# Kernel optimization log

Hardware: AMD Instinct MI355X
Metric: run time of the kernel (lower is better)

The kernel has to match this reference:

```python
import jax, jax.numpy as jnp
import numpy as np

R = 3                 # search_radius
S2 = (2 * R + 1) ** 2  # 49 correlation channels
VIS_PIXEL_SCALE = 0.1  # arcsec / pixel


def _interp_tokens(tokens, sh, sw, dh, dw):
    # tokens [B, N, D] on (sh, sw) grid -> (dh, dw) grid
    B, N, D = tokens.shape
    x = jnp.transpose(tokens, (0, 2, 1)).reshape(B, D, sh, sw)
    if (sh, sw) != (dh, dw):
        # torch F.interpolate bilinear align_corners=False == jax half-pixel bilinear
        x = jax.image.resize(x, (B, D, dh, dw), method='bilinear')
    return x  # [B, D, dh, dw]


def _l2norm(x, eps=1e-12):
    n = jnp.sqrt(jnp.sum(x * x, axis=1, keepdims=True))
    return x / jnp.maximum(n, eps)


def _corr_volume(q, ref):
    # q, ref: [B, D, H, W]; local cosine-similarity volume [B, S2, H, W]
    q = _l2norm(q)
    ref = _l2norm(ref)
    B, D, H, W = q.shape
    refp = jnp.pad(ref, ((0, 0), (0, 0), (R, R), (R, R)), mode='edge')  # replicate pad
    slices = [
        jnp.sum(q * jax.lax.dynamic_slice(refp, (0, 0, R + dy, R + dx), (B, D, H, W)), axis=1)
        for dy in range(-R, R + 1) for dx in range(-R, R + 1)
    ]
    return jnp.stack(slices, axis=1)


def _conv5(x, w, b):
    y = jax.lax.conv_general_dilated(x, w, (1, 1), 'SAME',
                                     dimension_numbers=('NCHW', 'OIHW', 'NCHW'))
    return y + b[None, :, None, None]


def _refine_net(x, w0, b0, w1, b1, w2, b2):
    h = jax.nn.gelu(_conv5(x, w0, b0), approximate=False)
    h = jax.nn.gelu(_conv5(h, w1, b1), approximate=False)
    return _conv5(h, w2, b2)


def setup_inputs() -> dict:
    key = jax.random.key(0)
    ks = jax.random.split(key, 8)
    B, D = 4, 256
    rubin_tokens = jax.random.normal(ks[0], (B, 64 * 64, D), dtype=jnp.float32)
    vis_tokens = jax.random.normal(ks[1], (B, 128 * 128, D), dtype=jnp.float32)
    in_ch = 2 + S2 + 1  # 52
    hid = 32
    def kaiming(k, shape):
        fan_in = shape[1] * shape[2] * shape[3]
        return jax.random.normal(k, shape, dtype=jnp.float32) / np.sqrt(fan_in)
    w0 = kaiming(ks[2], (hid, in_ch, 5, 5)); b0 = jnp.zeros((hid,), jnp.float32)
    w1 = kaiming(ks[3], (hid, hid, 5, 5));   b1 = jnp.zeros((hid,), jnp.float32)
    w2 = kaiming(ks[4], (2, hid, 5, 5));     b2 = jnp.zeros((2,), jnp.float32)
    log_temp = jnp.asarray(np.log(0.1), dtype=jnp.float32)
    return {
        'rubin_tokens': rubin_tokens, 'vis_tokens': vis_tokens,
        'w0': w0, 'b0': b0, 'w1': w1, 'b1': b1, 'w2': w2, 'b2': b2,
        'log_temp': log_temp,
        'rubin_h': 64, 'rubin_w': 64, 'vis_h': 128, 'vis_w': 128,
        'img_h': 2048, 'img_w': 2048,
    }


def reference(rubin_tokens, vis_tokens, w0, b0, w1, b1, w2, b2, log_temp,
              rubin_h, rubin_w, vis_h, vis_w, img_h, img_w):
    Hc, Wc = max(rubin_h, vis_h), max(rubin_w, vis_w)
    q = _interp_tokens(rubin_tokens, rubin_h, rubin_w, Hc, Wc)  # [B,D,Hc,Wc]
    k = _interp_tokens(vis_tokens, vis_h, vis_w, Hc, Wc)
    corr = _corr_volume(q, k)  # [B,S2,Hc,Wc]

    # soft-argmax over the (2R+1)^2 neighborhood
    coords = jnp.arange(-R, R + 1, dtype=corr.dtype)
    cy, cx = jnp.meshgrid(coords, coords, indexing='ij')
    cy = cy.reshape(1, S2, 1, 1)
    cx = cx.reshape(1, S2, 1, 1)
    temp = jnp.exp(log_temp)
    weights = jax.nn.softmax(corr / temp, axis=1)
    dy = jnp.sum(weights * cy, axis=1, keepdims=True)
    dx = jnp.sum(weights * cx, axis=1, keepdims=True)
    confidence = jnp.max(weights, axis=1, keepdims=True)
    raw_offsets = jnp.concatenate([dy, dx], axis=1)  # [B,2,Hc,Wc]

    x = jnp.concatenate([raw_offsets, corr, confidence], axis=1)  # [B,52,Hc,Wc]
    residual = _refine_net(x, w0, b0, w1, b1, w2, b2)
    refined = raw_offsets + residual

    sky_per_token_y = img_h * VIS_PIXEL_SCALE / Hc
    sky_per_token_x = img_w * VIS_PIXEL_SCALE / Wc
    dra = refined[:, 1:2] * sky_per_token_x
    ddec = refined[:, 0:1] * sky_per_token_y
    # [B,5,Hc,Wc]: dra, ddec, raw_dy, raw_dx, confidence
    return jnp.concatenate([dra, ddec, dy, dx, confidence], axis=1)
```

## Files before the change

kernel.cpp:

```cpp
#include <hip/hip_runtime.h>
#include <math.h>

#define Hh 128
#define Ww 128
#define Dd 256
#define Bb 4
#define HW (Hh*Ww)
#define NPIX (Bb*HW)
#define WP 132

typedef __attribute__((ext_vector_type(8))) short s16x8;
typedef __attribute__((ext_vector_type(4))) float f32x4;

__device__ __forceinline__ unsigned short f2bf(float f) {
    unsigned u = __float_as_uint(f);
    u += 0x7FFF + ((u >> 16) & 1);
    return (unsigned short)(u >> 16);
}

__device__ __forceinline__ float gelu_exact(float v) {
    return 0.5f * v * (1.0f + erff(v * 0.70710678118654752f));
}

#define ZGRAN 1115136
__global__ __launch_bounds__(256) void setup_fill(const float* __restrict__ w0,
                                                  const float* __restrict__ w1,
                                                  const float* __restrict__ w2,
                                                  unsigned short* __restrict__ wb0,
                                                  unsigned short* __restrict__ wb1,
                                                  unsigned short* __restrict__ wb2,
                                                  uint4* __restrict__ zbase) {
    int t = blockIdx.x * 256 + threadIdx.x;
    if (t < ZGRAN) {
        zbase[t] = (uint4){0, 0, 0, 0};
        return;
    }
    int u = t - ZGRAN;
    if (u < 51200) {
        int tap = u >> 11; int r = u & 2047; int n = r >> 6; int k = r & 63;
        wb0[u] = (k < 52) ? f2bf(w0[n * 1300 + k * 25 + tap]) : (unsigned short)0;
    } else if (u < 76800) {
        int v = u - 51200; int tap = v >> 10; int r = v & 1023; int n = r >> 5; int k = r & 31;
        wb1[v] = f2bf(w1[n * 800 + k * 25 + tap]);
    } else if (u < 89600) {
        int v = u - 76800; int tap = v >> 9; int r = v & 511; int n = r >> 5; int k = r & 31;
        wb2[v] = (n < 2) ? f2bf(w2[n * 800 + k * 25 + tap]) : (unsigned short)0;
    }
}

__global__ __launch_bounds__(256) void norm_fused(const float* __restrict__ vis,
                                                  const float* __restrict__ rub,
                                                  unsigned short* __restrict__ kn,
                                                  unsigned short* __restrict__ qn) {
    int tid = threadIdx.x;
    int g16 = tid >> 4, l = tid & 15;
    int blk = blockIdx.x;
    if (blk < 4096) {
        int pix = blk * 16 + g16;
        const float* base = vis + (size_t)pix * Dd + l * 4;
        float4 v[4];
#pragma unroll
        for (int i = 0; i < 4; i++) v[i] = *(const float4*)(base + i * 64);
        float ss = 0.f;
#pragma unroll
        for (int i = 0; i < 4; i++)
            ss += v[i].x * v[i].x + v[i].y * v[i].y + v[i].z * v[i].z + v[i].w * v[i].w;
#pragma unroll
        for (int o = 1; o <= 8; o <<= 1) ss += __shfl_xor(ss, o, 64);
        float inv = __builtin_amdgcn_rsqf(fmaxf(ss, 1e-24f));
        unsigned short* op = kn + (size_t)pix * Dd + l * 4;
#pragma unroll
        for (int i = 0; i < 4; i++) {
            ushort4 o4;
            o4.x = f2bf(v[i].x * inv); o4.y = f2bf(v[i].y * inv);
            o4.z = f2bf(v[i].z * inv); o4.w = f2bf(v[i].w * inv);
            *(ushort4*)(op + i * 64) = o4;
        }
    } else {
        int pix = (blk - 4096) * 16 + g16;
        int b = pix >> 14; int yx = pix & 16383; int y = yx >> 7; int x = yx & 127;
        float sy = 0.5f * y - 0.25f;
        float sx = 0.5f * x - 0.25f;
        int y0 = (int)floorf(sy); float fy = sy - (float)y0;
        int x0 = (int)floorf(sx); float fx = sx - (float)x0;
        int y0c = max(y0, 0), y1c = min(y0 + 1, 63);
        int x0c = max(x0, 0), x1c = min(x0 + 1, 63);
        const float* base = rub + (size_t)b * 4096 * Dd + l * 4;
        const float* p00 = base + (size_t)(y0c * 64 + x0c) * Dd;
        const float* p01 = base + (size_t)(y0c * 64 + x1c) * Dd;
        const float* p10 = base + (size_t)(y1c * 64 + x0c) * Dd;
        const float* p11 = base + (size_t)(y1c * 64 + x1c) * Dd;
        float w00 = (1.f - fy) * (1.f - fx), w01 = (1.f - fy) * fx;
        float w10 = fy * (1.f - fx), w11 = fy * fx;
        float4 bv[4];
        float ss = 0.f;
#pragma unroll
        for (int i = 0; i < 4; i++) {
            float4 a = *(const float4*)(p00 + i * 64);
            float4 b1 = *(const float4*)(p01 + i * 64);
            float4 c = *(const float4*)(p10 + i * 64);
            float4 d = *(const float4*)(p11 + i * 64);
            float4 v;
            v.x = w00 * a.x + w01 * b1.x + w10 * c.x + w11 * d.x;
            v.y = w00 * a.y + w01 * b1.y + w10 * c.y + w11 * d.y;
            v.z = w00 * a.z + w01 * b1.z + w10 * c.z + w11 * d.z;
            v.w = w00 * a.w + w01 * b1.w + w10 * c.w + w11 * d.w;
            bv[i] = v;
            ss += v.x * v.x + v.y * v.y + v.z * v.z + v.w * v.w;
        }
#pragma unroll
        for (int o = 1; o <= 8; o <<= 1) ss += __shfl_xor(ss, o, 64);
        float inv = __builtin_amdgcn_rsqf(fmaxf(ss, 1e-24f));
        unsigned short* op = qn + (size_t)pix * Dd + l * 4;
#pragma unroll
        for (int i = 0; i < 4; i++) {
            ushort4 o4;
            o4.x = f2bf(bv[i].x * inv); o4.y = f2bf(bv[i].y * inv);
            o4.z = f2bf(bv[i].z * inv); o4.w = f2bf(bv[i].w * inv);
            *(ushort4*)(op + i * 64) = o4;
        }
    }
}

__global__ __launch_bounds__(1024) void corr_block(const unsigned short* __restrict__ qn,
                                                   const unsigned short* __restrict__ kn,
                                                   const float* __restrict__ log_temp,
                                                   unsigned short* __restrict__ xb,
                                                   float* __restrict__ out) {
    __shared__ char smem[484 * 5 * 16];
    int tid = threadIdx.x;
    int wid = tid >> 6, lane = tid & 63, l15 = lane & 15, quad = lane >> 4;
    int blk = blockIdx.x;
    int b = blk >> 6, rem = blk & 63;
    int y0 = ((rem >> 3) & 7) << 4, x0 = (rem & 7) << 4;
    int y = y0 + wid;

    const unsigned short* src0; int dst0;
    const unsigned short* src1 = nullptr; int dst1 = 0;
    bool hav1;
    {
        int g = tid;
        int px = g >> 2, sub = g & 3;
        int ry = px / 22, rx = px - ry * 22;
        int yy = min(max(y0 - 3 + ry, 0), 127);
        int xx = min(max(x0 - 3 + rx, 0), 127);
        src0 = kn + ((size_t)(b << 14) + yy * 128 + xx) * 256 + sub * 8;
        dst0 = (px * 5 + sub) * 16;
        g = 1024 + tid;
        hav1 = (g < 1936);
        int gc = hav1 ? g : 1935;
        px = gc >> 2; sub = gc & 3;
        ry = px / 22; rx = px - ry * 22;
        yy = min(max(y0 - 3 + ry, 0), 127);
        xx = min(max(x0 - 3 + rx, 0), 127);
        src1 = kn + ((size_t)(b << 14) + yy * 128 + xx) * 256 + sub * 8;
        dst1 = (px * 5 + sub) * 16;
    }
    int lpixoff[10];
#pragma unroll
    for (int f = 0; f < 10; f++) {
        int p = min(f * 16 + l15, 153);
        int pr = p / 22, pc = p - pr * 22;
        lpixoff[f] = (((wid + pr) * 22 + pc) * 5 + quad) * 16;
    }
    const unsigned short* aptr = qn + ((size_t)(b << 14) + y * 128 + x0 + l15) * 256 + quad * 8;

    f32x4 acc[10];
#pragma unroll
    for (int f = 0; f < 10; f++) acc[f] = (f32x4){0.f, 0.f, 0.f, 0.f};

    uint4 v0 = *(const uint4*)src0;
    uint4 v1 = *(const uint4*)src1;
    s16x8 an = *(const s16x8*)aptr;
    for (int c = 0; c < 8; c++) {
        uint4 w0v = v0, w1v = v1;
        s16x8 a = an;
        if (c < 7) {
            v0 = *(const uint4*)(src0 + (c + 1) * 32);
            v1 = *(const uint4*)(src1 + (c + 1) * 32);
            an = *(const s16x8*)(aptr + (c + 1) * 32);
        }
        __syncthreads();
        *(uint4*)(smem + dst0) = w0v;
        if (hav1) *(uint4*)(smem + dst1) = w1v;
        __syncthreads();
#pragma unroll
        for (int f = 0; f < 10; f++) {
            s16x8 bf = *(const s16x8*)(smem + lpixoff[f]);
            acc[f] = __builtin_amdgcn_mfma_f32_16x16x32_bf16(a, bf, acc[f], 0, 0, 0);
        }
    }

    float inv_temp = expf(-log_temp[0]);
    float vmax[4] = {-1e30f, -1e30f, -1e30f, -1e30f};
#pragma unroll
    for (int f = 0; f < 10; f++) {
        int n = f * 16 + l15;
        if (n <= 153) {
            int dy = n / 22 - 3;
            int rx = n - (dy + 3) * 22;
#pragma unroll
            for (int i = 0; i < 4; i++) {
                int m = quad * 4 + i;
                int dx = rx - m - 3;
                if ((unsigned)(dx + 3) <= 6u) vmax[i] = fmaxf(vmax[i], acc[f][i]);
            }
        }
    }
#pragma unroll
    for (int o = 1; o <= 8; o <<= 1) {
#pragma unroll
        for (int i = 0; i < 4; i++) vmax[i] = fmaxf(vmax[i], __shfl_xor(vmax[i], o, 64));
    }
    float se[4] = {0, 0, 0, 0}, sey[4] = {0, 0, 0, 0}, sex[4] = {0, 0, 0, 0}, emax[4] = {0, 0, 0, 0};
    unsigned short* xrow = xb + ((size_t)(b * WP + y + 2) * WP + x0 + 2) * 64;
#pragma unroll
    for (int f = 0; f < 10; f++) {
        int n = f * 16 + l15;
        if (n <= 153) {
            int dy = n / 22 - 3;
            int rx = n - (dy + 3) * 22;
#pragma unroll
            for (int i = 0; i < 4; i++) {
                int m = quad * 4 + i;
                int dx = rx - m - 3;
                if ((unsigned)(dx + 3) <= 6u) {
                    float v = acc[f][i];
                    float e = expf((v - vmax[i]) * inv_temp);
                    se[i] += e;
                    sey[i] += e * (float)dy;
                    sex[i] += e * (float)dx;
                    emax[i] = fmaxf(emax[i], e);
                    xrow[(size_t)m * 64 + 2 + (dy + 3) * 7 + (dx + 3)] = f2bf(v);
                }
            }
        }
    }
#pragma unroll
    for (int o = 1; o <= 8; o <<= 1) {
#pragma unroll
        for (int i = 0; i < 4; i++) {
            se[i] += __shfl_xor(se[i], o, 64);
            sey[i] += __shfl_xor(sey[i], o, 64);
            sex[i] += __shfl_xor(sex[i], o, 64);
            emax[i] = fmaxf(emax[i], __shfl_xor(emax[i], o, 64));
        }
    }
    if (l15 == 0) {
#pragma unroll
        for (int i = 0; i < 4; i++) {
            int m = quad * 4 + i;
            float inv_se = 1.0f / se[i];
            float dyv = sey[i] * inv_se, dxv = sex[i] * inv_se, conf = emax[i] * inv_se;
            unsigned short* xp = xrow + (size_t)m * 64;
            xp[0] = f2bf(dyv); xp[1] = f2bf(dxv); xp[51] = f2bf(conf);
            float* op = out + (size_t)b * 5 * HW + y * 128 + x0 + m;
            op[2 * HW] = dyv; op[3 * HW] = dxv; op[4 * HW] = conf;
        }
    }
}

template <int KS, int OC, bool GELU>
__global__ __launch_bounds__(1024) void conv_tile(const unsigned short* __restrict__ in,
                                                  const unsigned short* __restrict__ wb,
                                                  const float* __restrict__ bias,
                                                  unsigned short* __restrict__ outp) {
    constexpr int ICP = KS * 32;
    constexpr int NF = OC / 16;
    constexpr int ABYTES = 400 * 5 * 16;
    constexpr int WBYTES = 5 * OC * 5 * 16;
    __shared__ char smem[ABYTES + WBYTES];
    int tid = threadIdx.x;
    int wv = tid >> 6, lane = tid & 63, l15 = lane & 15, quad = lane >> 4;
    int blk = blockIdx.x;
    int b = blk >> 6, ty = (blk >> 3) & 7, tx = blk & 7;
    int y0 = ty * 16, x0 = tx * 16;

    f32x4 acc[NF];
#pragma unroll
    for (int g = 0; g < NF; g++) acc[g] = (f32x4){0.f, 0.f, 0.f, 0.f};

    for (int ks = 0; ks < KS; ks++) {
        __syncthreads();
#pragma unroll
        for (int i = 0; i < 2; i++) {
            int g = i * 1024 + tid;
            if (g < 1600) {
                int px = g >> 2, sub = g & 3;
                int r = px / 20, c = px - r * 20;
                *(uint4*)(smem + (px * 5 + sub) * 16) =
                    *(const uint4*)(in + ((size_t)(b * WP + y0 + r) * WP + x0 + c) * ICP + ks * 32 + sub * 8);
            }
        }
        for (int ky = 0; ky < 5; ky++) {
            if (ky > 0) __syncthreads();
            constexpr int WGR = 5 * OC * 4;
#pragma unroll
            for (int i = 0; i < (WGR + 1023) / 1024; i++) {
                int g = i * 1024 + tid;
                if (g < WGR) {
                    int nl = g >> 2, sub = g & 3;
                    *(uint4*)(smem + ABYTES + (nl * 5 + sub) * 16) =
                        *(const uint4*)(wb + ((size_t)(ky * 5 * OC) + nl) * ICP + ks * 32 + sub * 8);
                }
            }
            __syncthreads();
#pragma unroll
            for (int kx = 0; kx < 5; kx++) {
                int abyte = (((wv + ky) * 20 + l15 + kx) * 5 + quad) * 16;
                s16x8 a = *(const s16x8*)(smem + abyte);
#pragma unroll
                for (int g = 0; g < NF; g++) {
                    int wbyte = ABYTES + ((kx * OC + g * 16 + l15) * 5 + quad) * 16;
                    s16x8 bf = *(const s16x8*)(smem + wbyte);
                    acc[g] = __builtin_amdgcn_mfma_f32_16x16x32_bf16(a, bf, acc[g], 0, 0, 0);
                }
            }
        }
    }
    size_t orow = ((size_t)(b * WP + y0 + wv + 2) * WP + x0 + 2) * OC;
#pragma unroll
    for (int g = 0; g < NF; g++) {
        float bv = bias[g * 16 + l15];
#pragma unroll
        for (int r = 0; r < 4; r++) {
            int m = quad * 4 + r;
            float v = acc[g][r] + bv;
            if (GELU) v = gelu_exact(v);
            outp[orow + (size_t)m * OC + g * 16 + l15] = f2bf(v);
        }
    }
}

__global__ __launch_bounds__(1024) void conv_final_tile(const unsigned short* __restrict__ in,
                                                        const unsigned short* __restrict__ wb,
                                                        const float* __restrict__ bias,
                                                        float* __restrict__ out) {
    constexpr int ICP = 32, OC = 16;
    constexpr int ABYTES = 400 * 5 * 16;
    constexpr int WBYTES = 5 * OC * 5 * 16;
    __shared__ char smem[ABYTES + WBYTES];
    int tid = threadIdx.x;
    int wv = tid >> 6, lane = tid & 63, l15 = lane & 15, quad = lane >> 4;
    int blk = blockIdx.x;
    int b = blk >> 6, ty = (blk >> 3) & 7, tx = blk & 7;
    int y0 = ty * 16, x0 = tx * 16;

    f32x4 acc = (f32x4){0.f, 0.f, 0.f, 0.f};
    __syncthreads();
#pragma unroll
    for (int i = 0; i < 2; i++) {
        int g = i * 1024 + tid;
        if (g < 1600) {
            int px = g >> 2, sub = g & 3;
            int r = px / 20, c = px - r * 20;
            *(uint4*)(smem + (px * 5 + sub) * 16) =
                *(const uint4*)(in + ((size_t)(b * WP + y0 + r) * WP + x0 + c) * ICP + sub * 8);
        }
    }
    for (int ky = 0; ky < 5; ky++) {
        if (ky > 0) __syncthreads();
        constexpr int WGR = 5 * OC * 4;
        {
            int g = tid;
            if (g < WGR) {
                int nl = g >> 2, sub = g & 3;
                *(uint4*)(smem + ABYTES + (nl * 5 + sub) * 16) =
                    *(const uint4*)(wb + ((size_t)(ky * 5 * OC) + nl) * ICP + sub * 8);
            }
        }
        __syncthreads();
#pragma unroll
        for (int kx = 0; kx < 5; kx++) {
            int abyte = (((wv + ky) * 20 + l15 + kx) * 5 + quad) * 16;
            s16x8 a = *(const s16x8*)(smem + abyte);
            int wbyte = ABYTES + ((kx * OC + l15) * 5 + quad) * 16;
            s16x8 bf = *(const s16x8*)(smem + wbyte);
            acc = __builtin_amdgcn_mfma_f32_16x16x32_bf16(a, bf, acc, 0, 0, 0);
        }
    }
    if (l15 < 2) {
        float bv = bias[l15];
#pragma unroll
        for (int r = 0; r < 4; r++) {
            int m = quad * 4 + r;
            size_t p5 = (size_t)b * 5 * HW + (y0 + wv) * Ww + x0 + m;
            float a = acc[r] + bv;
            if (l15 == 0) {
                float dyv = out[p5 + 2 * HW];
                out[p5 + HW] = (dyv + a) * 1.6f;
            } else {
                float dxv = out[p5 + 3 * HW];
                out[p5] = (dxv + a) * 1.6f;
            }
        }
    }
}

extern "C" void kernel_launch(void* const* d_in, const int* in_sizes, int n_in,
                              void* d_out, int out_size, void* d_ws, size_t ws_size,
                              hipStream_t stream) {
    const float* rub = (const float*)d_in[0];
    const float* vis = (const float*)d_in[1];
    const float* w0 = (const float*)d_in[2];
    const float* b0 = (const float*)d_in[3];
    const float* w1 = (const float*)d_in[4];
    const float* b1 = (const float*)d_in[5];
    const float* w2 = (const float*)d_in[6];
    const float* b2 = (const float*)d_in[7];
    const float* log_temp = (const float*)d_in[8];
    float* out = (float*)d_out;

    char* ws = (char*)d_ws;
    size_t off = 0;
    const size_t PADPIX = (size_t)Bb * WP * WP;
    unsigned short* kn = (unsigned short*)(ws + off); off += (size_t)NPIX * Dd * 2;
    unsigned short* qn = (unsigned short*)(ws + off); off += (size_t)NPIX * Dd * 2;
    unsigned short* xbp = (unsigned short*)(ws + off); off += PADPIX * 64 * 2;
    unsigned short* h1p = (unsigned short*)(ws + off); off += PADPIX * 32 * 2;
    unsigned short* h2p = (unsigned short*)(ws + off); off += PADPIX * 32 * 2;
    unsigned short* wb0 = (unsigned short*)(ws + off); off += 51200 * 2;
    unsigned short* wb1 = (unsigned short*)(ws + off); off += 25600 * 2;
    unsigned short* wb2 = (unsigned short*)(ws + off); off += 12800 * 2;

    setup_fill<<<4706, 256, 0, stream>>>(w0, w1, w2, wb0, wb1, wb2, (uint4*)xbp);
    norm_fused<<<8192, 256, 0, stream>>>(vis, rub, kn, qn);
    corr_block<<<256, 1024, 0, stream>>>(qn, kn, log_temp, xbp, out);
    conv_tile<2, 32, true><<<256, 1024, 0, stream>>>(xbp, wb0, b0, h1p);
    conv_tile<1, 32, true><<<256, 1024, 0, stream>>>(h1p, wb1, b1, h2p);
    conv_final_tile<<<256, 1024, 0, stream>>>(h2p, wb2, b2, out);
}
```

Measured before the change: 216.1 us.

## Fuse three refine convolutions into one halo-recompute pyramid kernel

Replaces the three separate conv kernels with one kernel per 16x16 tile. It loads a 28x28 halo of the correlation features, computes conv1 on 24x24 and conv2 on 20x20 in shared memory, then runs the final conv, with XOR-swizzled LDS layouts. The padded border grows from 2 to 6 so the larger halo can be read, and the h1/h2 global buffers go away. This removes two launches and the global round-trips of the intermediate activations, at the cost of recomputing halo pixels (about 2.25x the conv1 work) and much larger shared memory per block.

```diff
diff --git a/kernel.cpp b/kernel.cpp
--- a/kernel.cpp
+++ b/kernel.cpp
@@ -7,7 +7,7 @@
 #define Bb 4
 #define HW (Hh*Ww)
 #define NPIX (Bb*HW)
-#define WP 132
+#define WP 140
 
 typedef __attribute__((ext_vector_type(8))) short s16x8;
 typedef __attribute__((ext_vector_type(4))) float f32x4;
@@ -22,7 +22,7 @@
     return 0.5f * v * (1.0f + erff(v * 0.70710678118654752f));
 }
 
-#define ZGRAN 1115136
+#define ZGRAN 627200
 __global__ __launch_bounds__(256) void setup_fill(const float* __restrict__ w0,
                                                   const float* __restrict__ w1,
                                                   const float* __restrict__ w2,
@@ -213,7 +213,7 @@
         for (int i = 0; i < 4; i++) vmax[i] = fmaxf(vmax[i], __shfl_xor(vmax[i], o, 64));
     }
     float se[4] = {0, 0, 0, 0}, sey[4] = {0, 0, 0, 0}, sex[4] = {0, 0, 0, 0}, emax[4] = {0, 0, 0, 0};
-    unsigned short* xrow = xb + ((size_t)(b * WP + y + 2) * WP + x0 + 2) * 64;
+    unsigned short* xrow = xb + ((size_t)(b * WP + y + 6) * WP + x0 + 6) * 64;
 #pragma unroll
     for (int f = 0; f < 10; f++) {
         int n = f * 16 + l15;
@@ -260,138 +260,204 @@
     }
 }
 
-template <int KS, int OC, bool GELU>
-__global__ __launch_bounds__(1024) void conv_tile(const unsigned short* __restrict__ in,
-                                                  const unsigned short* __restrict__ wb,
-                                                  const float* __restrict__ bias,
-                                                  unsigned short* __restrict__ outp) {
-    constexpr int ICP = KS * 32;
-    constexpr int NF = OC / 16;
-    constexpr int ABYTES = 400 * 5 * 16;
-    constexpr int WBYTES = 5 * OC * 5 * 16;
-    __shared__ char smem[ABYTES + WBYTES];
+__global__ __launch_bounds__(1024) void conv_pyramid(const unsigned short* __restrict__ xb,
+                                                     const unsigned short* __restrict__ wb0,
+                                                     const float* __restrict__ b0,
+                                                     const unsigned short* __restrict__ wb1,
+                                                     const float* __restrict__ b1,
+                                                     const unsigned short* __restrict__ wb2,
+                                                     const float* __restrict__ b2,
+                                                     float* __restrict__ out) {
+    constexpr int XBYTES = 784 * 64;
+    constexpr int WBYTES = 13 * 32 * 64;
+    constexpr int H1BYTES = 576 * 64;
+    constexpr int H2BYTES = 400 * 64;
+    __shared__ char smem[XBYTES + WBYTES + H1BYTES + H2BYTES];
+    char* sX = smem;
+    char* sW = smem + XBYTES;
+    char* sH1 = smem + XBYTES + WBYTES;
+    char* sH2 = sH1 + H1BYTES;
+
     int tid = threadIdx.x;
     int wv = tid >> 6, lane = tid & 63, l15 = lane & 15, quad = lane >> 4;
     int blk = blockIdx.x;
     int b = blk >> 6, ty = (blk >> 3) & 7, tx = blk & 7;
     int y0 = ty * 16, x0 = tx * 16;
 
-    f32x4 acc[NF];
-#pragma unroll
-    for (int g = 0; g < NF; g++) acc[g] = (f32x4){0.f, 0.f, 0.f, 0.f};
-
-    for (int ks = 0; ks < KS; ks++) {
-        __syncthreads();
-#pragma unroll
-        for (int i = 0; i < 2; i++) {
+    auto stage_x = [&](int ks) {
+#pragma unroll
+        for (int i = 0; i < 4; i++) {
             int g = i * 1024 + tid;
-            if (g < 1600) {
+            if (g < 3136) {
                 int px = g >> 2, sub = g & 3;
-                int r = px / 20, c = px - r * 20;
-                *(uint4*)(smem + (px * 5 + sub) * 16) =
-                    *(const uint4*)(in + ((size_t)(b * WP + y0 + r) * WP + x0 + c) * ICP + ks * 32 + sub * 8);
-            }
-        }
-        for (int ky = 0; ky < 5; ky++) {
-            if (ky > 0) __syncthreads();
-            constexpr int WGR = 5 * OC * 4;
-#pragma unroll
-            for (int i = 0; i < (WGR + 1023) / 1024; i++) {
-                int g = i * 1024 + tid;
-                if (g < WGR) {
-                    int nl = g >> 2, sub = g & 3;
-                    *(uint4*)(smem + ABYTES + (nl * 5 + sub) * 16) =
-                        *(const uint4*)(wb + ((size_t)(ky * 5 * OC) + nl) * ICP + ks * 32 + sub * 8);
+                int r = px / 28, c = px - r * 28;
+                *(uint4*)(sX + px * 64 + ((sub ^ ((px >> 1) & 3)) << 4)) =
+                    *(const uint4*)(xb + ((size_t)(b * WP + y0 + r) * WP + x0 + c) * 64 + ks * 32 + sub * 8);
+            }
+        }
+    };
+    auto stage_w = [&](const unsigned short* src, int rows, int rlen, int choff) {
+        int ngr = rows * 4;
+        for (int i = 0; i * 1024 < ngr; i++) {
+            int g = i * 1024 + tid;
+            if (g < ngr) {
+                int nl = g >> 2, sub = g & 3;
+                *(uint4*)(sW + nl * 64 + ((sub ^ ((nl >> 1) & 3)) << 4)) =
+                    *(const uint4*)(src + (size_t)nl * rlen + choff + sub * 8);
+            }
+        }
+    };
+
+    f32x4 acc1[3][2];
+#pragma unroll
+    for (int s = 0; s < 3; s++) { acc1[s][0] = (f32x4){0,0,0,0}; acc1[s][1] = (f32x4){0,0,0,0}; }
+
+    auto conv1_half = [&](int tap0, int nt) {
+        for (int t = 0; t < nt; t++) {
+            int tap = tap0 + t;
+            int ky = tap / 5, kx = tap - ky * 5;
+            int lr0 = t * 32 + l15;
+            s16x8 wf0 = *(const s16x8*)(sW + lr0 * 64 + ((quad ^ ((lr0 >> 1) & 3)) << 4));
+            int lr1 = lr0 + 16;
+            s16x8 wf1 = *(const s16x8*)(sW + lr1 * 64 + ((quad ^ ((lr1 >> 1) & 3)) << 4));
+#pragma unroll
+            for (int s = 0; s < 3; s++) {
+                int u = s * 16 + wv;
+                int r = u >> 1, cb = (u & 1) << 4;
+                int px = (r + ky) * 28 + min(cb + l15 + kx, 27);
+                s16x8 a = *(const s16x8*)(sX + px * 64 + ((quad ^ ((px >> 1) & 3)) << 4));
+                acc1[s][0] = __builtin_amdgcn_mfma_f32_16x16x32_bf16(a, wf0, acc1[s][0], 0, 0, 0);
+                acc1[s][1] = __builtin_amdgcn_mfma_f32_16x16x32_bf16(a, wf1, acc1[s][1], 0, 0, 0);
+            }
+        }
+    };
+
+    stage_x(0); stage_w(wb0, 13 * 32, 64, 0);
+    __syncthreads();
+    conv1_half(0, 13);
+    __syncthreads();
+    stage_w(wb0 + 13 * 32 * 64, 12 * 32, 64, 0);
+    __syncthreads();
+    conv1_half(13, 12);
+    __syncthreads();
+    stage_x(1); stage_w(wb0, 13 * 32, 64, 32);
+    __syncthreads();
+    conv1_half(0, 13);
+    __syncthreads();
+    stage_w(wb0 + 13 * 32 * 64, 12 * 32, 64, 32);
+    __syncthreads();
+    conv1_half(13, 12);
+
+#pragma unroll
+    for (int s = 0; s < 3; s++) {
+        int u = s * 16 + wv;
+        int r = u >> 1, cb = (u & 1) << 4;
+        int ay = y0 + r - 4;
+#pragma unroll
+        for (int g = 0; g < 2; g++) {
+            float bv = b0[g * 16 + l15];
+#pragma unroll
+            for (int rr = 0; rr < 4; rr++) {
+                int col = cb + quad * 4 + rr;
+                if (col < 24) {
+                    float v = gelu_exact(acc1[s][g][rr] + bv);
+                    int ax = x0 + col - 4;
+                    unsigned short o = ((unsigned)ay < 128u && (unsigned)ax < 128u) ? f2bf(v)
+                                                                                    : (unsigned short)0;
+                    int px = r * 24 + col;
+                    int gran = g * 2 + (l15 >> 3);
+                    *(unsigned short*)(sH1 + px * 64 + ((gran ^ ((px >> 1) & 3)) << 4) + (l15 & 7) * 2) = o;
                 }
             }
-            __syncthreads();
-#pragma unroll
-            for (int kx = 0; kx < 5; kx++) {
-                int abyte = (((wv + ky) * 20 + l15 + kx) * 5 + quad) * 16;
-                s16x8 a = *(const s16x8*)(smem + abyte);
-#pragma unroll
-                for (int g = 0; g < NF; g++) {
-                    int wbyte = ABYTES + ((kx * OC + g * 16 + l15) * 5 + quad) * 16;
-                    s16x8 bf = *(const s16x8*)(smem + wbyte);
-                    acc[g] = __builtin_amdgcn_mfma_f32_16x16x32_bf16(a, bf, acc[g], 0, 0, 0);
+        }
+    }
+    __syncthreads();
+
+    f32x4 acc2[3][2];
+#pragma unroll
+    for (int s = 0; s < 3; s++) { acc2[s][0] = (f32x4){0,0,0,0}; acc2[s][1] = (f32x4){0,0,0,0}; }
+
+    auto conv2_half = [&](int tap0, int nt) {
+        for (int t = 0; t < nt; t++) {
+            int tap = tap0 + t;
+            int ky = tap / 5, kx = tap - ky * 5;
+            int lr0 = t * 32 + l15;
+            s16x8 wf0 = *(const s16x8*)(sW + lr0 * 64 + ((quad ^ ((lr0 >> 1) & 3)) << 4));
+            int lr1 = lr0 + 16;
+            s16x8 wf1 = *(const s16x8*)(sW + lr1 * 64 + ((quad ^ ((lr1 >> 1) & 3)) << 4));
+#pragma unroll
+            for (int s = 0; s < 3; s++) {
+                int u = s * 16 + wv;
+                if (u < 40) {
+                    int r = u >> 1, cb = (u & 1) << 4;
+                    int px = (r + ky) * 24 + min(cb + l15 + kx, 23);
+                    s16x8 a = *(const s16x8*)(sH1 + px * 64 + ((quad ^ ((px >> 1) & 3)) << 4));
+                    acc2[s][0] = __builtin_amdgcn_mfma_f32_16x16x32_bf16(a, wf0, acc2[s][0], 0, 0, 0);
+                    acc2[s][1] = __builtin_amdgcn_mfma_f32_16x16x32_bf16(a, wf1, acc2[s][1], 0, 0, 0);
                 }
             }
         }
-    }
-    size_t orow = ((size_t)(b * WP + y0 + wv + 2) * WP + x0 + 2) * OC;
-#pragma unroll
-    for (int g = 0; g < NF; g++) {
-        float bv = bias[g * 16 + l15];
-#pragma unroll
-        for (int r = 0; r < 4; r++) {
-            int m = quad * 4 + r;
-            float v = acc[g][r] + bv;
-            if (GELU) v = gelu_exact(v);
-            outp[orow + (size_t)m * OC + g * 16 + l15] = f2bf(v);
-        }
-    }
-}
-
-__global__ __launch_bounds__(1024) void conv_final_tile(const unsigned short* __restrict__ in,
-                                                        const unsigned short* __restrict__ wb,
-                                                        const float* __restrict__ bias,
-                                                        float* __restrict__ out) {
-    constexpr int ICP = 32, OC = 16;
-    constexpr int ABYTES = 400 * 5 * 16;
-    constexpr int WBYTES = 5 * OC * 5 * 16;
-    __shared__ char smem[ABYTES + WBYTES];
-    int tid = threadIdx.x;
-    int wv = tid >> 6, lane = tid & 63, l15 = lane & 15, quad = lane >> 4;
-    int blk = blockIdx.x;
-    int b = blk >> 6, ty = (blk >> 3) & 7, tx = blk & 7;
-    int y0 = ty * 16, x0 = tx * 16;
-
-    f32x4 acc = (f32x4){0.f, 0.f, 0.f, 0.f};
-    __syncthreads();
-#pragma unroll
-    for (int i = 0; i < 2; i++) {
-        int g = i * 1024 + tid;
-        if (g < 1600) {
-            int px = g >> 2, sub = g & 3;
-            int r = px / 20, c = px - r * 20;
-            *(uint4*)(smem + (px * 5 + sub) * 16) =
-                *(const uint4*)(in + ((size_t)(b * WP + y0 + r) * WP + x0 + c) * ICP + sub * 8);
-        }
-    }
-    for (int ky = 0; ky < 5; ky++) {
-        if (ky > 0) __syncthreads();
-        constexpr int WGR = 5 * OC * 4;
-        {
-            int g = tid;
-            if (g < WGR) {
-                int nl = g >> 2, sub = g & 3;
-                *(uint4*)(smem + ABYTES + (nl * 5 + sub) * 16) =
-                    *(const uint4*)(wb + ((size_t)(ky * 5 * OC) + nl) * ICP + sub * 8);
-            }
-        }
-        __syncthreads();
-#pragma unroll
-        for (int kx = 0; kx < 5; kx++) {
-            int abyte = (((wv + ky) * 20 + l15 + kx) * 5 + quad) * 16;
-            s16x8 a = *(const s16x8*)(smem + abyte);
-            int wbyte = ABYTES + ((kx * OC + l15) * 5 + quad) * 16;
-            s16x8 bf = *(const s16x8*)(smem + wbyte);
-            acc = __builtin_amdgcn_mfma_f32_16x16x32_bf16(a, bf, acc, 0, 0, 0);
-        }
-    }
+    };
+
+    stage_w(wb1, 13 * 32, 32, 0);
+    __syncthreads();
+    conv2_half(0, 13);
+    __syncthreads();
+    stage_w(wb1 + 13 * 32 * 32, 12 * 32, 32, 0);
+    __syncthreads();
+    conv2_half(13, 12);
+
+#pragma unroll
+    for (int s = 0; s < 3; s++) {
+        int u = s * 16 + wv;
+        if (u < 40) {
+            int r = u >> 1, cb = (u & 1) << 4;
+            int ay = y0 + r - 2;
+#pragma unroll
+            for (int g = 0; g < 2; g++) {
+                float bv = b1[g * 16 + l15];
+#pragma unroll
+                for (int rr = 0; rr < 4; rr++) {
+                    int col = cb + quad * 4 + rr;
+                    if (col < 20) {
+                        float v = gelu_exact(acc2[s][g][rr] + bv);
+                        int ax = x0 + col - 2;
+                        unsigned short o = ((unsigned)ay < 128u && (unsigned)ax < 128u) ? f2bf(v)
+                                                                                        : (unsigned short)0;
+                        int px = r * 20 + col;
+                        int gran = g * 2 + (l15 >> 3);
+                        *(unsigned short*)(sH2 + px * 64 + ((gran ^ ((px >> 1) & 3)) << 4) + (l15 & 7) * 2) = o;
+                    }
+                }
+            }
+        }
+    }
+    __syncthreads();
+
+    stage_w(wb2, 400, 32, 0);
+    __syncthreads();
+
+    f32x4 acc3 = (f32x4){0, 0, 0, 0};
+    for (int t = 0; t < 25; t++) {
+        int ky = t / 5, kx = t - ky * 5;
+        int px = (wv + ky) * 20 + l15 + kx;
+        s16x8 a = *(const s16x8*)(sH2 + px * 64 + ((quad ^ ((px >> 1) & 3)) << 4));
+        int lr = t * 16 + l15;
+        s16x8 wf = *(const s16x8*)(sW + lr * 64 + ((quad ^ ((lr >> 1) & 3)) << 4));
+        acc3 = __builtin_amdgcn_mfma_f32_16x16x32_bf16(a, wf, acc3, 0, 0, 0);
+    }
+
     if (l15 < 2) {
-        float bv = bias[l15];
-#pragma unroll
-        for (int r = 0; r < 4; r++) {
-            int m = quad * 4 + r;
+        float bv = b2[l15];
+#pragma unroll
+        for (int rr = 0; rr < 4; rr++) {
+            int m = quad * 4 + rr;
             size_t p5 = (size_t)b * 5 * HW + (y0 + wv) * Ww + x0 + m;
-            float a = acc[r] + bv;
+            float a = acc3[rr] + bv;
             if (l15 == 0) {
-                float dyv = out[p5 + 2 * HW];
-                out[p5 + HW] = (dyv + a) * 1.6f;
+                out[p5 + HW] = (out[p5 + 2 * HW] + a) * 1.6f;
             } else {
-                float dxv = out[p5 + 3 * HW];
-                out[p5] = (dxv + a) * 1.6f;
+                out[p5] = (out[p5 + 3 * HW] + a) * 1.6f;
             }
         }
     }
@@ -417,16 +483,12 @@
     unsigned short* kn = (unsigned short*)(ws + off); off += (size_t)NPIX * Dd * 2;
     unsigned short* qn = (unsigned short*)(ws + off); off += (size_t)NPIX * Dd * 2;
     unsigned short* xbp = (unsigned short*)(ws + off); off += PADPIX * 64 * 2;
-    unsigned short* h1p = (unsigned short*)(ws + off); off += PADPIX * 32 * 2;
-    unsigned short* h2p = (unsigned short*)(ws + off); off += PADPIX * 32 * 2;
     unsigned short* wb0 = (unsigned short*)(ws + off); off += 51200 * 2;
     unsigned short* wb1 = (unsigned short*)(ws + off); off += 25600 * 2;
     unsigned short* wb2 = (unsigned short*)(ws + off); off += 12800 * 2;
 
-    setup_fill<<<4706, 256, 0, stream>>>(w0, w1, w2, wb0, wb1, wb2, (uint4*)xbp);
+    setup_fill<<<2800, 256, 0, stream>>>(w0, w1, w2, wb0, wb1, wb2, (uint4*)xbp);
     norm_fused<<<8192, 256, 0, stream>>>(vis, rub, kn, qn);
     corr_block<<<256, 1024, 0, stream>>>(qn, kn, log_temp, xbp, out);
-    conv_tile<2, 32, true><<<256, 1024, 0, stream>>>(xbp, wb0, b0, h1p);
-    conv_tile<1, 32, true><<<256, 1024, 0, stream>>>(h1p, wb1, b1, h2p);
-    conv_final_tile<<<256, 1024, 0, stream>>>(h2p, wb2, b2, out);
-}
+    conv_pyramid<<<256, 1024, 0, stream>>>(xbp, wb0, b0, wb1, b1, wb2, b2, out);
+}
```

Result: slower. 248.2 us (+14.8%).

## Stage rubin tokens in LDS for upsample and halve spatial tiles across kernels

Applied to the files above, without the earlier changes.

Each rubin-upsample block now loads a 6x6 token patch (with clamped borders) into shared memory once and computes an 8x8 patch of bilinear-interpolated, normalized outputs from LDS. Before, every output pixel issued four global float4 gathers. The correlation and conv kernels switch from 16x16 tiles with 1024 threads to 8x16 tiles with 512 threads. That doubles the grid to 512 blocks so more of the CUs are busy and several blocks can share a CU. The smaller tiles add halo overhead per output pixel, and the norm kernel's new 37 KB shared buffer is also allocated by the vis-normalization blocks, which may cut their occupancy.

```diff
diff --git a/kernel.cpp b/kernel.cpp
--- a/kernel.cpp
+++ b/kernel.cpp
@@ -52,6 +52,7 @@
                                                   const float* __restrict__ rub,
                                                   unsigned short* __restrict__ kn,
                                                   unsigned short* __restrict__ qn) {
+    __shared__ float stok[36 * 260];
     int tid = threadIdx.x;
     int g16 = tid >> 4, l = tid & 15;
     int blk = blockIdx.x;
@@ -77,67 +78,85 @@
             *(ushort4*)(op + i * 64) = o4;
         }
     } else {
-        int pix = (blk - 4096) * 16 + g16;
-        int b = pix >> 14; int yx = pix & 16383; int y = yx >> 7; int x = yx & 127;
-        float sy = 0.5f * y - 0.25f;
-        float sx = 0.5f * x - 0.25f;
-        int y0 = (int)floorf(sy); float fy = sy - (float)y0;
-        int x0 = (int)floorf(sx); float fx = sx - (float)x0;
-        int y0c = max(y0, 0), y1c = min(y0 + 1, 63);
-        int x0c = max(x0, 0), x1c = min(x0 + 1, 63);
-        const float* base = rub + (size_t)b * 4096 * Dd + l * 4;
-        const float* p00 = base + (size_t)(y0c * 64 + x0c) * Dd;
-        const float* p01 = base + (size_t)(y0c * 64 + x1c) * Dd;
-        const float* p10 = base + (size_t)(y1c * 64 + x0c) * Dd;
-        const float* p11 = base + (size_t)(y1c * 64 + x1c) * Dd;
-        float w00 = (1.f - fy) * (1.f - fx), w01 = (1.f - fy) * fx;
-        float w10 = fy * (1.f - fx), w11 = fy * fx;
-        float4 bv[4];
-        float ss = 0.f;
-#pragma unroll
-        for (int i = 0; i < 4; i++) {
-            float4 a = *(const float4*)(p00 + i * 64);
-            float4 b1 = *(const float4*)(p01 + i * 64);
-            float4 c = *(const float4*)(p10 + i * 64);
-            float4 d = *(const float4*)(p11 + i * 64);
-            float4 v;
-            v.x = w00 * a.x + w01 * b1.x + w10 * c.x + w11 * d.x;
-            v.y = w00 * a.y + w01 * b1.y + w10 * c.y + w11 * d.y;
-            v.z = w00 * a.z + w01 * b1.z + w10 * c.z + w11 * d.z;
-            v.w = w00 * a.w + w01 * b1.w + w10 * c.w + w11 * d.w;
-            bv[i] = v;
-            ss += v.x * v.x + v.y * v.y + v.z * v.z + v.w * v.w;
-        }
-#pragma unroll
-        for (int o = 1; o <= 8; o <<= 1) ss += __shfl_xor(ss, o, 64);
-        float inv = __builtin_amdgcn_rsqf(fmaxf(ss, 1e-24f));
-        unsigned short* op = qn + (size_t)pix * Dd + l * 4;
-#pragma unroll
-        for (int i = 0; i < 4; i++) {
-            ushort4 o4;
-            o4.x = f2bf(bv[i].x * inv); o4.y = f2bf(bv[i].y * inv);
-            o4.z = f2bf(bv[i].z * inv); o4.w = f2bf(bv[i].w * inv);
-            *(ushort4*)(op + i * 64) = o4;
-        }
-    }
-}
-
-__global__ __launch_bounds__(1024) void corr_block(const unsigned short* __restrict__ qn,
-                                                   const unsigned short* __restrict__ kn,
-                                                   const float* __restrict__ log_temp,
-                                                   unsigned short* __restrict__ xb,
-                                                   float* __restrict__ out) {
-    __shared__ char smem[484 * 5 * 16];
+        int blk2 = blk - 4096;
+        int b = blk2 >> 8;
+        int rem = blk2 & 255;
+        int ty = rem >> 4, tx = rem & 15;
+        int oy0 = ty * 8, ox0 = tx * 8;
+        int rb = ty * 4 - 1, cb = tx * 4 - 1;
+#pragma unroll
+        for (int i = 0; i < 9; i++) {
+            int g = i * 256 + tid;
+            int t = g >> 6, c = g & 63;
+            int jy = t / 6, jx = t - jy * 6;
+            int gy = min(max(rb + jy, 0), 63);
+            int gx = min(max(cb + jx, 0), 63);
+            *(float4*)&stok[t * 260 + c * 4] =
+                *(const float4*)(rub + ((size_t)(b * 4096 + gy * 64 + gx)) * 256 + c * 4);
+        }
+        __syncthreads();
+        for (int k = 0; k < 4; k++) {
+            int pp = g16 * 4 + k;
+            int r = pp >> 3, c2 = pp & 7;
+            int yo = oy0 + r, xo = ox0 + c2;
+            float sy = 0.5f * yo - 0.25f, sx = 0.5f * xo - 0.25f;
+            float fyf = floorf(sy), fxf = floorf(sx);
+            float fy = sy - fyf, fx = sx - fxf;
+            int jy0 = (int)fyf - rb, jx0 = (int)fxf - cb;
+            const float* t00 = &stok[(jy0 * 6 + jx0) * 260 + l * 4];
+            const float* t01 = t00 + 260;
+            const float* t10 = t00 + 6 * 260;
+            const float* t11 = t10 + 260;
+            float w00 = (1.f - fy) * (1.f - fx), w01 = (1.f - fy) * fx;
+            float w10 = fy * (1.f - fx), w11 = fy * fx;
+            float4 bv[4];
+            float ss = 0.f;
+#pragma unroll
+            for (int i = 0; i < 4; i++) {
+                float4 a = *(const float4*)(t00 + i * 64);
+                float4 b1 = *(const float4*)(t01 + i * 64);
+                float4 c = *(const float4*)(t10 + i * 64);
+                float4 d = *(const float4*)(t11 + i * 64);
+                float4 v;
+                v.x = w00 * a.x + w01 * b1.x + w10 * c.x + w11 * d.x;
+                v.y = w00 * a.y + w01 * b1.y + w10 * c.y + w11 * d.y;
+                v.z = w00 * a.z + w01 * b1.z + w10 * c.z + w11 * d.z;
+                v.w = w00 * a.w + w01 * b1.w + w10 * c.w + w11 * d.w;
+                bv[i] = v;
+                ss += v.x * v.x + v.y * v.y + v.z * v.z + v.w * v.w;
+            }
+#pragma unroll
+            for (int o = 1; o <= 8; o <<= 1) ss += __shfl_xor(ss, o, 64);
+            float inv = __builtin_amdgcn_rsqf(fmaxf(ss, 1e-24f));
+            size_t pix = (size_t)(b << 14) + yo * 128 + xo;
+            unsigned short* op = qn + pix * Dd + l * 4;
+#pragma unroll
+            for (int i = 0; i < 4; i++) {
+                ushort4 o4;
+                o4.x = f2bf(bv[i].x * inv); o4.y = f2bf(bv[i].y * inv);
+                o4.z = f2bf(bv[i].z * inv); o4.w = f2bf(bv[i].w * inv);
+                *(ushort4*)(op + i * 64) = o4;
+            }
+        }
+    }
+}
+
+__global__ __launch_bounds__(512, 4) void corr_block(const unsigned short* __restrict__ qn,
+                                                     const unsigned short* __restrict__ kn,
+                                                     const float* __restrict__ log_temp,
+                                                     unsigned short* __restrict__ xb,
+                                                     float* __restrict__ out) {
+    __shared__ char smem[308 * 5 * 16];
     int tid = threadIdx.x;
     int wid = tid >> 6, lane = tid & 63, l15 = lane & 15, quad = lane >> 4;
     int blk = blockIdx.x;
-    int b = blk >> 6, rem = blk & 63;
-    int y0 = ((rem >> 3) & 7) << 4, x0 = (rem & 7) << 4;
+    int b = blk >> 7, rem = blk & 127;
+    int y0 = (rem >> 3) << 3, x0 = (rem & 7) << 4;
     int y = y0 + wid;
 
     const unsigned short* src0; int dst0;
-    const unsigned short* src1 = nullptr; int dst1 = 0;
-    bool hav1;
+    const unsigned short* src1; int dst1;
+    const unsigned short* src2; int dst2; bool hav2;
     {
         int g = tid;
         int px = g >> 2, sub = g & 3;
@@ -146,15 +165,22 @@
         int xx = min(max(x0 - 3 + rx, 0), 127);
         src0 = kn + ((size_t)(b << 14) + yy * 128 + xx) * 256 + sub * 8;
         dst0 = (px * 5 + sub) * 16;
-        g = 1024 + tid;
-        hav1 = (g < 1936);
-        int gc = hav1 ? g : 1935;
-        px = gc >> 2; sub = gc & 3;
+        g = 512 + tid;
+        px = g >> 2; sub = g & 3;
         ry = px / 22; rx = px - ry * 22;
         yy = min(max(y0 - 3 + ry, 0), 127);
         xx = min(max(x0 - 3 + rx, 0), 127);
         src1 = kn + ((size_t)(b << 14) + yy * 128 + xx) * 256 + sub * 8;
         dst1 = (px * 5 + sub) * 16;
+        g = 1024 + tid;
+        hav2 = (g < 1232);
+        int gc = hav2 ? g : 1231;
+        px = gc >> 2; sub = gc & 3;
+        ry = px / 22; rx = px - ry * 22;
+        yy = min(max(y0 - 3 + ry, 0), 127);
+        xx = min(max(x0 - 3 + rx, 0), 127);
+        src2 = kn + ((size_t)(b << 14) + yy * 128 + xx) * 256 + sub * 8;
+        dst2 = (px * 5 + sub) * 16;
     }
     int lpixoff[10];
 #pragma unroll
@@ -171,18 +197,21 @@
 
     uint4 v0 = *(const uint4*)src0;
     uint4 v1 = *(const uint4*)src1;
+    uint4 v2 = *(const uint4*)src2;
     s16x8 an = *(const s16x8*)aptr;
     for (int c = 0; c < 8; c++) {
-        uint4 w0v = v0, w1v = v1;
+        uint4 w0v = v0, w1v = v1, w2v = v2;
         s16x8 a = an;
         if (c < 7) {
             v0 = *(const uint4*)(src0 + (c + 1) * 32);
             v1 = *(const uint4*)(src1 + (c + 1) * 32);
+            v2 = *(const uint4*)(src2 + (c + 1) * 32);
             an = *(const s16x8*)(aptr + (c + 1) * 32);
         }
         __syncthreads();
         *(uint4*)(smem + dst0) = w0v;
-        if (hav1) *(uint4*)(smem + dst1) = w1v;
+        *(uint4*)(smem + dst1) = w1v;
+        if (hav2) *(uint4*)(smem + dst2) = w2v;
         __syncthreads();
 #pragma unroll
         for (int f = 0; f < 10; f++) {
@@ -261,20 +290,21 @@
 }
 
 template <int KS, int OC, bool GELU>
-__global__ __launch_bounds__(1024) void conv_tile(const unsigned short* __restrict__ in,
-                                                  const unsigned short* __restrict__ wb,
-                                                  const float* __restrict__ bias,
-                                                  unsigned short* __restrict__ outp) {
+__global__ __launch_bounds__(512, 4) void conv_tile(const unsigned short* __restrict__ in,
+                                                    const unsigned short* __restrict__ wb,
+                                                    const float* __restrict__ bias,
+                                                    unsigned short* __restrict__ outp) {
     constexpr int ICP = KS * 32;
     constexpr int NF = OC / 16;
-    constexpr int ABYTES = 400 * 5 * 16;
+    constexpr int ABYTES = 240 * 5 * 16;
     constexpr int WBYTES = 5 * OC * 5 * 16;
     __shared__ char smem[ABYTES + WBYTES];
     int tid = threadIdx.x;
     int wv = tid >> 6, lane = tid & 63, l15 = lane & 15, quad = lane >> 4;
     int blk = blockIdx.x;
-    int b = blk >> 6, ty = (blk >> 3) & 7, tx = blk & 7;
-    int y0 = ty * 16, x0 = tx * 16;
+    int b = blk >> 7, rem = blk & 127;
+    int ty = rem >> 3, tx = rem & 7;
+    int y0 = ty * 8, x0 = tx * 16;
 
     f32x4 acc[NF];
 #pragma unroll
@@ -284,8 +314,8 @@
         __syncthreads();
 #pragma unroll
         for (int i = 0; i < 2; i++) {
-            int g = i * 1024 + tid;
-            if (g < 1600) {
+            int g = i * 512 + tid;
+            if (g < 960) {
                 int px = g >> 2, sub = g & 3;
                 int r = px / 20, c = px - r * 20;
                 *(uint4*)(smem + (px * 5 + sub) * 16) =
@@ -296,8 +326,8 @@
             if (ky > 0) __syncthreads();
             constexpr int WGR = 5 * OC * 4;
 #pragma unroll
-            for (int i = 0; i < (WGR + 1023) / 1024; i++) {
-                int g = i * 1024 + tid;
+            for (int i = 0; i < (WGR + 511) / 512; i++) {
+                int g = i * 512 + tid;
                 if (g < WGR) {
                     int nl = g >> 2, sub = g & 3;
                     *(uint4*)(smem + ABYTES + (nl * 5 + sub) * 16) =
@@ -332,26 +362,26 @@
     }
 }
 
-__global__ __launch_bounds__(1024) void conv_final_tile(const unsigned short* __restrict__ in,
-                                                        const unsigned short* __restrict__ wb,
-                                                        const float* __restrict__ bias,
-                                                        float* __restrict__ out) {
+__global__ __launch_bounds__(512, 4) void conv_final_tile(const unsigned short* __restrict__ in,
+                                                          const unsigned short* __restrict__ wb,
+                                                          const float* __restrict__ bias,
+                                                          float* __restrict__ out) {
     constexpr int ICP = 32, OC = 16;
-    constexpr int ABYTES = 400 * 5 * 16;
+    constexpr int ABYTES = 240 * 5 * 16;
     constexpr int WBYTES = 5 * OC * 5 * 16;
     __shared__ char smem[ABYTES + WBYTES];
     int tid = threadIdx.x;
     int wv = tid >> 6, lane = tid & 63, l15 = lane & 15, quad = lane >> 4;
     int blk = blockIdx.x;
-    int b = blk >> 6, ty = (blk >> 3) & 7, tx = blk & 7;
-    int y0 = ty * 16, x0 = tx * 16;
+    int b = blk >> 7, rem = blk & 127;
+    int ty = rem >> 3, tx = rem & 7;
+    int y0 = ty * 8, x0 = tx * 16;
 
     f32x4 acc = (f32x4){0.f, 0.f, 0.f, 0.f};
-    __syncthreads();
 #pragma unroll
     for (int i = 0; i < 2; i++) {
-        int g = i * 1024 + tid;
-        if (g < 1600) {
+        int g = i * 512 + tid;
+        if (g < 960) {
             int px = g >> 2, sub = g & 3;
             int r = px / 20, c = px - r * 20;
             *(uint4*)(smem + (px * 5 + sub) * 16) =
@@ -424,9 +454,9 @@
     unsigned short* wb2 = (unsigned short*)(ws + off); off += 12800 * 2;
 
     setup_fill<<<4706, 256, 0, stream>>>(w0, w1, w2, wb0, wb1, wb2, (uint4*)xbp);
-    norm_fused<<<8192, 256, 0, stream>>>(vis, rub, kn, qn);
-    corr_block<<<256, 1024, 0, stream>>>(qn, kn, log_temp, xbp, out);
-    conv_tile<2, 32, true><<<256, 1024, 0, stream>>>(xbp, wb0, b0, h1p);
-    conv_tile<1, 32, true><<<256, 1024, 0, stream>>>(h1p, wb1, b1, h2p);
-    conv_final_tile<<<256, 1024, 0, stream>>>(h2p, wb2, b2, out);
-}
+    norm_fused<<<5120, 256, 0, stream>>>(vis, rub, kn, qn);
+    corr_block<<<512, 512, 0, stream>>>(qn, kn, log_temp, xbp, out);
+    conv_tile<2, 32, true><<<512, 512, 0, stream>>>(xbp, wb0, b0, h1p);
+    conv_tile<1, 32, true><<<512, 512, 0, stream>>>(h1p, wb1, b1, h2p);
+    conv_final_tile<<<512, 512, 0, stream>>>(h2p, wb2, b2, out);
+}
```

Result: faster. 206.6 us (-4.4%).
